# Performance work log

Measured on AMD Instinct MI355X. Metric: run time of the kernel, lower is better.

## Reference

```python
import jax, jax.numpy as jnp
import numpy as np

B, T, C, H = 2, 2048, 1024, 16
D = C // H  # head dim = 64
EPS = 1e-5


def _layernorm(x, g, b):
    mu = jnp.mean(x, axis=-1, keepdims=True)
    var = jnp.mean((x - mu) ** 2, axis=-1, keepdims=True)
    return (x - mu) * jax.lax.rsqrt(var + EPS) * g + b


def setup_inputs() -> dict:
    key = jax.random.key(0)
    ks = jax.random.split(key, 16)
    s = 1.0 / np.sqrt(C)
    inp = {
        "x": jax.random.normal(ks[0], (B, T, C), dtype=jnp.float32),
        "Wq": jax.random.normal(ks[1], (C, C), dtype=jnp.float32) * s,
        "bq": jnp.zeros((C,), jnp.float32),
        "Wk": jax.random.normal(ks[2], (C, C), dtype=jnp.float32) * s,
        "bk": jnp.zeros((C,), jnp.float32),
        "Wv": jax.random.normal(ks[3], (C, C), dtype=jnp.float32) * s,
        "bv": jnp.zeros((C,), jnp.float32),
        "Wo": jax.random.normal(ks[4], (C, C), dtype=jnp.float32) * s,
        "bo": jnp.zeros((C,), jnp.float32),
        "ln1_g": jnp.ones((C,), jnp.float32),
        "ln1_b": jnp.zeros((C,), jnp.float32),
        "ln2_g": jnp.ones((C,), jnp.float32),
        "ln2_b": jnp.zeros((C,), jnp.float32),
        "W1": jax.random.normal(ks[5], (C, 4 * C), dtype=jnp.float32) * s,
        "b1": jnp.zeros((4 * C,), jnp.float32),
        "W2": jax.random.normal(ks[6], (4 * C, C), dtype=jnp.float32) * (1.0 / np.sqrt(4 * C)),
        "b2": jnp.zeros((C,), jnp.float32),
    }
    return inp


def _block(x, Wq, bq, Wk, bk, Wv, bv, Wo, bo, ln1_g, ln1_b, ln2_g, ln2_b, W1, b1, W2, b2):
    # --- attention sublayer (pre-LN, residual) ---
    h = _layernorm(x, ln1_g, ln1_b)
    q = (h @ Wq + bq).reshape(B, T, H, D)
    k = (h @ Wk + bk).reshape(B, T, H, D)
    v = (h @ Wv + bv).reshape(B, T, H, D)
    scores = jnp.einsum("bthd,bshd->bhts", q, k) * (1.0 / np.sqrt(D))
    attn = jax.nn.softmax(scores, axis=-1)  # dropout is identity at eval
    y = jnp.einsum("bhts,bshd->bthd", attn, v).reshape(B, T, C)
    x = x + (y @ Wo + bo)
    # --- MLP sublayer (pre-LN, residual) ---
    h2 = _layernorm(x, ln2_g, ln2_b)
    m = jax.nn.gelu(h2 @ W1 + b1, approximate=False)  # torch nn.GELU() is exact erf
    x = x + (m @ W2 + b2)
    return x


def reference(x, Wq, bq, Wk, bk, Wv, bv, Wo, bo, ln1_g, ln1_b, ln2_g, ln2_b, W1, b1, W2, b2):
    return _block(x, Wq, bq, Wk, bk, Wv, bv, Wo, bo, ln1_g, ln1_b, ln2_g, ln2_b, W1, b1, W2, b2)
```

## Files before the change

kernel.cpp:

```cpp
#include <hip/hip_runtime.h>
#include <math.h>

typedef unsigned short u16;
typedef unsigned int   u32;
using bf16x8 = __attribute__((ext_vector_type(8))) short;
using f32x4  = __attribute__((ext_vector_type(4))) float;
using f32x16 = __attribute__((ext_vector_type(16))) float;

static constexpr int Bb = 2, Tt = 2048, Cc = 1024, Hh = 16, Dd = 64;
static constexpr int QS = 3072;
static constexpr float QSCALE = 0.125f * 1.44269504089f;

__device__ __forceinline__ u16 f2bf(float f){
  u32 u = __builtin_bit_cast(u32, f);
  u += 0x7fffu + ((u >> 16) & 1u);
  return (u16)(u >> 16);
}
__device__ __forceinline__ float bf2f(u16 v){
  u32 u = (u32)v << 16;
  return __builtin_bit_cast(float, u);
}

__device__ __forceinline__ void gl2lds16(const void* g, void* l){
  __builtin_amdgcn_global_load_lds((const __attribute__((address_space(1))) void*)g,
                                   (__attribute__((address_space(3))) void*)l, 16, 0, 0);
}

template<int N> __device__ __forceinline__ void waitvm(){
  if constexpr (N == 0) asm volatile("s_waitcnt vmcnt(0)" ::: "memory");
  else if constexpr (N == 3) asm volatile("s_waitcnt vmcnt(3)" ::: "memory");
  else if constexpr (N == 4) asm volatile("s_waitcnt vmcnt(4)" ::: "memory");
  else if constexpr (N == 6) asm volatile("s_waitcnt vmcnt(6)" ::: "memory");
  else if constexpr (N == 8) asm volatile("s_waitcnt vmcnt(8)" ::: "memory");
}

__device__ __forceinline__ void barrier_pin(){
  __builtin_amdgcn_s_barrier();
  __builtin_amdgcn_sched_barrier(0);
}

__device__ __forceinline__ f32x4 mfma16(bf16x8 a, bf16x8 b, f32x4 c){
  return __builtin_amdgcn_mfma_f32_16x16x32_bf16(a, b, c, 0, 0, 0);
}
__device__ __forceinline__ f32x16 mfma32(bf16x8 a, bf16x8 b, f32x16 c){
  return __builtin_amdgcn_mfma_f32_32x32x16_bf16(a, b, c, 0, 0, 0);
}

__device__ __forceinline__ float exp2f_fast(float x){
#if __has_builtin(__builtin_amdgcn_exp2f)
  return __builtin_amdgcn_exp2f(x);
#else
  return __expf(x * 0.69314718056f);
#endif
}

__device__ __forceinline__ float gelu_f(float x){
  return 0.5f * x * (1.0f + erff(x * 0.70710678118654752f));
}

__device__ __forceinline__ void plane_swap(u32& a, u32& b){
  asm("v_permlane32_swap_b32 %0, %1" : "+v"(a), "+v"(b));
}
__device__ __forceinline__ u32 cvtpk_bf16(float lo, float hi){
  u32 r;
  asm("v_cvt_pk_bf16_f32 %0, %1, %2" : "=v"(r) : "v"(lo), "v"(hi));
  return r;
}

__global__ __launch_bounds__(256) void ln_kernel(const float* __restrict__ x,
    const float* __restrict__ g, const float* __restrict__ b, u16* __restrict__ out)
{
  int row = blockIdx.x;
  int tid = threadIdx.x;
  const float4* xr = (const float4*)(x + (size_t)row * Cc);
  float4 v = xr[tid];
  float s  = v.x + v.y + v.z + v.w;
  float s2 = v.x*v.x + v.y*v.y + v.z*v.z + v.w*v.w;
  #pragma unroll
  for (int off = 1; off < 64; off <<= 1){ s += __shfl_xor(s, off); s2 += __shfl_xor(s2, off); }
  __shared__ float red[8];
  int wid = tid >> 6;
  if ((tid & 63) == 0){ red[wid] = s; red[4 + wid] = s2; }
  __syncthreads();
  s  = red[0] + red[1] + red[2] + red[3];
  s2 = red[4] + red[5] + red[6] + red[7];
  float mu   = s * (1.0f / Cc);
  float var  = s2 * (1.0f / Cc) - mu * mu;
  float rstd = rsqrtf(var + 1e-5f);
  const float4 gg = ((const float4*)g)[tid];
  const float4 bb = ((const float4*)b)[tid];
  ushort4 o;
  o.x = f2bf((v.x - mu) * rstd * gg.x + bb.x);
  o.y = f2bf((v.y - mu) * rstd * gg.y + bb.y);
  o.z = f2bf((v.z - mu) * rstd * gg.z + bb.z);
  o.w = f2bf((v.w - mu) * rstd * gg.w + bb.w);
  *(ushort4*)(out + (size_t)row * Cc + tid * 4) = o;
}

__global__ __launch_bounds__(256) void transpose_cast_kernel(const float* __restrict__ in,
    u16* __restrict__ out, int R, int Ccols)
{
  __shared__ float tile[32][33];
  int tx = threadIdx.x, ty = threadIdx.y;
  int c0 = blockIdx.x * 32, r0 = blockIdx.y * 32;
  #pragma unroll
  for (int j = 0; j < 4; j++) tile[ty + j*8][tx] = in[(size_t)(r0 + ty + j*8) * Ccols + c0 + tx];
  __syncthreads();
  #pragma unroll
  for (int j = 0; j < 4; j++) out[(size_t)(c0 + ty + j*8) * R + r0 + tx] = f2bf(tile[tx][ty + j*8]);
}

__global__ __launch_bounds__(256) void transpose4_kernel(
    const float* __restrict__ s0, const float* __restrict__ s1,
    const float* __restrict__ s2, const float* __restrict__ s3,
    u16* __restrict__ d0, u16* __restrict__ d1, u16* __restrict__ d2, u16* __restrict__ d3)
{
  __shared__ float tile[32][33];
  int z = blockIdx.z;
  const float* in = (z == 0) ? s0 : (z == 1) ? s1 : (z == 2) ? s2 : s3;
  u16* out        = (z == 0) ? d0 : (z == 1) ? d1 : (z == 2) ? d2 : d3;
  int tx = threadIdx.x, ty = threadIdx.y;
  int c0 = blockIdx.x * 32, r0 = blockIdx.y * 32;
  #pragma unroll
  for (int j = 0; j < 4; j++) tile[ty + j*8][tx] = in[(size_t)(r0 + ty + j*8) * 1024 + c0 + tx];
  __syncthreads();
  #pragma unroll
  for (int j = 0; j < 4; j++) out[(size_t)(c0 + ty + j*8) * 1024 + r0 + tx] = f2bf(tile[tx][ty + j*8]);
}

__global__ __launch_bounds__(256) void pack3_kernel(const float* __restrict__ a,
    const float* __restrict__ b, const float* __restrict__ c, float* __restrict__ o)
{
  int i = blockIdx.x * 256 + threadIdx.x;
  float v = (i < 1024) ? a[i] : (i < 2048 ? b[i - 1024] : c[i - 2048]);
  o[i] = v;
}

__global__ __launch_bounds__(256) void transpose_v_kernel(const u16* __restrict__ v, u16* __restrict__ vt)
{
  __shared__ u16 tile[32][33];
  int tx = threadIdx.x, ty = threadIdx.y;
  int bh = blockIdx.z; int b = bh >> 4, h = bh & 15;
  int t0 = blockIdx.x * 32, d0 = blockIdx.y * 32;
  const u16* src = v + (size_t)b * Tt * QS + h * Dd;
  #pragma unroll
  for (int j = 0; j < 4; j++) tile[ty + j*8][tx] = src[(size_t)(t0 + ty + j*8) * QS + d0 + tx];
  __syncthreads();
  u16* dst = vt + (size_t)bh * Dd * Tt;
  #pragma unroll
  for (int j = 0; j < 4; j++) dst[(size_t)(d0 + ty + j*8) * Tt + t0 + tx] = tile[tx][ty + j*8];
}

template<int BM, int BN, int WM, int WN, int WPEU, int EPI>
__global__ __launch_bounds__(WM * WN * 64, WPEU) void gemmc_kernel(
    const u16* __restrict__ A, const u16* __restrict__ BT,
    const float* __restrict__ bias, const float* __restrict__ resid,
    void* __restrict__ out, int K, int ldA, int ldOut)
{
  constexpr int THREADS = WM * WN * 64;
  constexpr int MF = (BM / WM) / 16;
  constexpr int NF = (BN / WN) / 16;
  constexpr int AG = (BM * 4) / THREADS;
  constexpr int BG = (BN * 4) / THREADS;
  constexpr int NLOADS = AG + BG;

  __shared__ alignas(16) u16 As[2][BM * 32];
  __shared__ alignas(16) u16 Bs[2][BN * 32];

  const int tid  = threadIdx.x;
  const int lane = tid & 63, wid = tid >> 6;
  const int l15  = lane & 15, lg = lane >> 4;

  const int gx  = gridDim.x;
  const int lin = blockIdx.x + gx * blockIdx.y;
  const int nwg = gx * gridDim.y;
  const int wl  = (lin & 7) * (nwg >> 3) + (lin >> 3);
  const int rowBase = (wl % gx) * BM, colBase = (wl / gx) * BN;

  const int wr = wid / WN, wc = wid % WN;

  f32x4 acc[MF][NF] = {};

  auto stage = [&](int buf, int k0){
    #pragma unroll
    for (int j = 0; j < AG; j++){
      int g = tid + THREADS * j;
      int row = g >> 2, p = g & 3;
      int w = p ^ (row & 3) ^ ((row >> 2) & 3);
      gl2lds16(A + (size_t)(rowBase + row) * ldA + k0 + w * 8, (u16*)As[buf] + g * 8);
    }
    #pragma unroll
    for (int j = 0; j < BG; j++){
      int g = tid + THREADS * j;
      int row = g >> 2, p = g & 3;
      int w = p ^ (row & 3) ^ ((row >> 2) & 3);
      gl2lds16(BT + (size_t)(colBase + row) * K + k0 + w * 8, (u16*)Bs[buf] + g * 8);
    }
  };

  stage(0, 0);
  const int nt = K >> 5;
  int cur = 0;
  for (int t = 0; t < nt; ++t, cur ^= 1){
    if (t + 1 < nt){ stage(cur ^ 1, (t + 1) << 5); waitvm<NLOADS>(); }
    else           { waitvm<0>(); }
    __builtin_amdgcn_s_barrier();
    __builtin_amdgcn_sched_barrier(0);

    const u16* Asb = (const u16*)As[cur];
    const u16* Bsb = (const u16*)Bs[cur];

    bf16x8 bfr[NF], afr[MF];
    #pragma unroll
    for (int ni = 0; ni < NF; ni++){
      int r = wc * (BN / WN) + ni * 16 + l15;
      bfr[ni] = *(const bf16x8*)(Bsb + r * 32 + ((lg ^ (r & 3) ^ ((r >> 2) & 3)) << 3));
    }
    #pragma unroll
    for (int mi = 0; mi < MF; mi++){
      int r = wr * (BM / WM) + mi * 16 + l15;
      afr[mi] = *(const bf16x8*)(Asb + r * 32 + ((lg ^ (r & 3) ^ ((r >> 2) & 3)) << 3));
    }
    __builtin_amdgcn_s_setprio(1);
    #pragma unroll
    for (int mi = 0; mi < MF; mi++)
      #pragma unroll
      for (int ni = 0; ni < NF; ni++)
        acc[mi][ni] = mfma16(afr[mi], bfr[ni], acc[mi][ni]);
    __builtin_amdgcn_s_setprio(0);

    __builtin_amdgcn_sched_barrier(0);
    __builtin_amdgcn_s_barrier();
  }

  #pragma unroll
  for (int mi = 0; mi < MF; mi++){
    #pragma unroll
    for (int ni = 0; ni < NF; ni++){
      int row = rowBase + wr * (BM / WM) + mi * 16 + lg * 4;
      int col = colBase + wc * (BN / WN) + ni * 16 + l15;
      float bc = bias[col];
      #pragma unroll
      for (int r = 0; r < 4; r++){
        float val = acc[mi][ni][r] + bc;
        size_t idx = (size_t)(row + r) * ldOut + col;
        if constexpr (EPI == 1)      ((float*)out)[idx] = val + resid[idx];
        else if constexpr (EPI == 2) ((u16*)out)[idx]   = f2bf(gelu_f(val));
        else if constexpr (EPI == 3) ((u16*)out)[idx]   = f2bf(col < 1024 ? val * QSCALE : val);
        else                         ((u16*)out)[idx]   = f2bf(val);
      }
    }
  }
}

__global__ __launch_bounds__(256, 4) void attn_kernel(const u16* __restrict__ q, const u16* __restrict__ k,
    const u16* __restrict__ vt, u16* __restrict__ opart, float* __restrict__ ml)
{
  __shared__ alignas(16) u16 Ks[2][64 * 64];
  __shared__ alignas(16) u16 Vs[2][64 * 64];
  int tid  = threadIdx.x;
  int lane = tid & 63, wid = tid >> 6;
  int l31  = lane & 31, hi = lane >> 5;

  int lin = blockIdx.x + 16 * blockIdx.y;
  int wl  = (lin & 7) * 64 + (lin >> 3);
  int qt  = wl & 15, bh = wl >> 4;
  int b = bh >> 4, h = bh & 15;
  int split = blockIdx.z;
  int kt0 = split * (Tt / 2);

  int qglob = qt * 128 + wid * 32 + l31;

  const u16* qp = q + ((size_t)b * Tt + qglob) * QS + h * Dd + hi * 8;
  bf16x8 qf[4];
  #pragma unroll
  for (int s = 0; s < 4; s++) qf[s] = *(const bf16x8*)(qp + s * 16);

  const u16* kbase = k  + (size_t)b * Tt * QS + h * Dd;
  const u16* vbase = vt + (size_t)bh * Dd * Tt;

  f32x16 yacc[2] = {};
  float m2 = -1e30f, lsum = 0.f;

  int g0 = tid, g1 = tid + 256;
  int r0 = g0 >> 3, cb0 = (g0 & 7) ^ (r0 & 7);
  int r1 = g1 >> 3, cb1 = (g1 & 7) ^ (r1 & 7);

  auto stageKV = [&](int buf, int kt){
    gl2lds16(kbase + (size_t)(kt + r0) * QS + cb0 * 8, (u16*)Ks[buf] + wid * 512);
    gl2lds16(kbase + (size_t)(kt + r1) * QS + cb1 * 8, (u16*)Ks[buf] + 2048 + wid * 512);
    gl2lds16(vbase + (size_t)r0 * Tt + kt + cb0 * 8,   (u16*)Vs[buf] + wid * 512);
    gl2lds16(vbase + (size_t)r1 * Tt + kt + cb1 * 8,   (u16*)Vs[buf] + 2048 + wid * 512);
  };

  stageKV(0, kt0);
  int cur = 0;
  for (int kt = kt0; kt < kt0 + Tt / 2; kt += 64) {
    if (kt + 64 < kt0 + Tt / 2) { stageKV(cur ^ 1, kt + 64); waitvm<4>(); }
    else                        { waitvm<0>(); }
    barrier_pin();

    const u16* Ksb = (const u16*)Ks[cur];
    const u16* Vsb = (const u16*)Vs[cur];
    int rx = l31 & 7;

    f32x16 st[2] = {};
    __builtin_amdgcn_s_setprio(1);
    #pragma unroll
    for (int nb = 0; nb < 2; nb++){
      const u16* krow = Ksb + (nb * 32 + l31) * 64;
      #pragma unroll
      for (int s = 0; s < 4; s++){
        bf16x8 kf = *(const bf16x8*)(krow + (((s * 2 + hi) ^ rx) << 3));
        st[nb] = mfma32(kf, qf[s], st[nb]);
      }
    }
    __builtin_amdgcn_s_setprio(0);

    float tm[16];
    #pragma unroll
    for (int i = 0; i < 16; i++) tm[i] = fmaxf(st[0][i], st[1][i]);
    #pragma unroll
    for (int w = 8; w; w >>= 1)
      #pragma unroll
      for (int i = 0; i < w; i++) tm[i] = fmaxf(tm[i], tm[i + w]);
    u32 ma = __builtin_bit_cast(u32, tm[0]), mb = ma;
    plane_swap(ma, mb);
    float mx = fmaxf(__builtin_bit_cast(float, ma), __builtin_bit_cast(float, mb));

    float mnew = fmaxf(m2, mx);
    float alpha = exp2f_fast(m2 - mnew);
    m2 = mnew;

    #pragma unroll
    for (int nb = 0; nb < 2; nb++)
      #pragma unroll
      for (int i = 0; i < 16; i++)
        st[nb][i] = exp2f_fast(st[nb][i] - m2);

    float ts[16];
    #pragma unroll
    for (int i = 0; i < 16; i++) ts[i] = st[0][i] + st[1][i];
    #pragma unroll
    for (int w = 8; w; w >>= 1)
      #pragma unroll
      for (int i = 0; i < w; i++) ts[i] += ts[i + w];
    u32 sa = __builtin_bit_cast(u32, ts[0]), sb = sa;
    plane_swap(sa, sb);
    lsum = lsum * alpha + __builtin_bit_cast(float, sa) + __builtin_bit_cast(float, sb);

    #pragma unroll
    for (int nd = 0; nd < 2; nd++)
      #pragma unroll
      for (int i = 0; i < 16; i++) yacc[nd][i] *= alpha;

    bf16x8 pb[4];
    #pragma unroll
    for (int nb = 0; nb < 2; nb++){
      u32 c[8];
      #pragma unroll
      for (int i = 0; i < 8; i++) c[i] = cvtpk_bf16(st[nb][2 * i], st[nb][2 * i + 1]);
      plane_swap(c[0], c[2]); plane_swap(c[1], c[3]);
      plane_swap(c[4], c[6]); plane_swap(c[5], c[7]);
      u32 f0[4] = {c[0], c[1], c[2], c[3]};
      u32 f1[4] = {c[4], c[5], c[6], c[7]};
      pb[nb * 2 + 0] = *(bf16x8*)f0;
      pb[nb * 2 + 1] = *(bf16x8*)f1;
    }

    __builtin_amdgcn_s_setprio(1);
    #pragma unroll
    for (int nd = 0; nd < 2; nd++){
      const u16* vrow = Vsb + (nd * 32 + l31) * 64;
      #pragma unroll
      for (int ks = 0; ks < 4; ks++){
        bf16x8 vf = *(const bf16x8*)(vrow + (((ks * 2 + hi) ^ rx) << 3));
        yacc[nd] = mfma32(vf, pb[ks], yacc[nd]);
      }
    }
    __builtin_amdgcn_s_setprio(0);

    __builtin_amdgcn_sched_barrier(0);
    barrier_pin();
    cur ^= 1;
  }

  float inv = 1.0f / lsum;
  u16* op = opart + ((size_t)split * (Bb * Tt) + (size_t)b * Tt + qglob) * Cc + h * Dd;
  #pragma unroll
  for (int nd = 0; nd < 2; nd++){
    #pragma unroll
    for (int g = 0; g < 4; g++){
      ushort4 o;
      o.x = f2bf(yacc[nd][g * 4 + 0] * inv);
      o.y = f2bf(yacc[nd][g * 4 + 1] * inv);
      o.z = f2bf(yacc[nd][g * 4 + 2] * inv);
      o.w = f2bf(yacc[nd][g * 4 + 3] * inv);
      *(ushort4*)(op + nd * 32 + g * 8 + hi * 4) = o;
    }
  }
  if (hi == 0){
    float* mlp = ml + (((size_t)split * (Bb * Tt) + (size_t)b * Tt + qglob) * Hh + h) * 2;
    mlp[0] = m2; mlp[1] = lsum;
  }
}

__global__ __launch_bounds__(256) void combine_kernel(const u16* __restrict__ opart,
    const float* __restrict__ ml, u16* __restrict__ y)
{
  int row = blockIdx.x;
  int d0  = threadIdx.x * 4;
  int h   = d0 >> 6;
  const float* p0 = ml + ((size_t)row * Hh + h) * 2;
  const float* p1 = ml + (((size_t)(Bb * Tt) + row) * Hh + h) * 2;
  float m0 = p0[0], l0 = p0[1], m1 = p1[0], l1 = p1[1];
  float M  = fmaxf(m0, m1);
  float u0 = l0 * exp2f_fast(m0 - M), u1 = l1 * exp2f_fast(m1 - M);
  float inv = 1.0f / (u0 + u1);
  float w0 = u0 * inv, w1 = u1 * inv;
  ushort4 a = *(const ushort4*)(opart + (size_t)row * Cc + d0);
  ushort4 c = *(const ushort4*)(opart + ((size_t)(Bb * Tt) + row) * Cc + d0);
  ushort4 o;
  o.x = f2bf(bf2f(a.x) * w0 + bf2f(c.x) * w1);
  o.y = f2bf(bf2f(a.y) * w0 + bf2f(c.y) * w1);
  o.z = f2bf(bf2f(a.z) * w0 + bf2f(c.z) * w1);
  o.w = f2bf(bf2f(a.w) * w0 + bf2f(c.w) * w1);
  *(ushort4*)(y + (size_t)row * Cc + d0) = o;
}

extern "C" void kernel_launch(void* const* d_in, const int* in_sizes, int n_in,
                              void* d_out, int out_size, void* d_ws, size_t ws_size,
                              hipStream_t stream)
{
  (void)in_sizes; (void)n_in; (void)out_size; (void)ws_size;
  const float* x    = (const float*)d_in[0];
  const float* Wq   = (const float*)d_in[1];
  const float* bq   = (const float*)d_in[2];
  const float* Wk   = (const float*)d_in[3];
  const float* bk   = (const float*)d_in[4];
  const float* Wv   = (const float*)d_in[5];
  const float* bv   = (const float*)d_in[6];
  const float* Wo   = (const float*)d_in[7];
  const float* bo   = (const float*)d_in[8];
  const float* ln1g = (const float*)d_in[9];
  const float* ln1b = (const float*)d_in[10];
  const float* ln2g = (const float*)d_in[11];
  const float* ln2b = (const float*)d_in[12];
  const float* W1   = (const float*)d_in[13];
  const float* b1   = (const float*)d_in[14];
  const float* W2   = (const float*)d_in[15];
  const float* b2   = (const float*)d_in[16];

  char* ws = (char*)d_ws;
  const size_t MB = 1024 * 1024;
  u16*   wqkvt = (u16*)(ws + 0 * MB);
  u16*   wot   = (u16*)(ws + 6 * MB);
  u16*   w1t   = (u16*)(ws + 8 * MB);
  u16*   w2t   = (u16*)(ws + 16 * MB);
  float* bqkv  = (float*)(ws + 24 * MB);
  u16*   hbuf  = (u16*)(ws + 25 * MB);
  u16*   qkv   = (u16*)(ws + 33 * MB);
  u16*   vtb   = (u16*)(ws + 57 * MB);
  u16*   yb    = (u16*)(ws + 65 * MB);
  u16*   opart = (u16*)(ws + 73 * MB);
  float* x2    = (float*)(ws + 73 * MB);
  float* mlb   = (float*)(ws + 89 * MB);
  u16*   h2    = hbuf;
  u16*   mb    = qkv;

  dim3 tb(32, 8);
  transpose4_kernel<<<dim3(32, 32, 4), tb, 0, stream>>>(Wq, Wk, Wv, Wo,
      wqkvt, wqkvt + 1024 * 1024, wqkvt + 2048 * 1024, wot);
  transpose_cast_kernel<<<dim3(128, 32), tb, 0, stream>>>(W1, w1t, 1024, 4096);
  transpose_cast_kernel<<<dim3(32, 128), tb, 0, stream>>>(W2, w2t, 4096, 1024);
  pack3_kernel<<<12, 256, 0, stream>>>(bq, bk, bv, bqkv);

  ln_kernel<<<4096, 256, 0, stream>>>(x, ln1g, ln1b, hbuf);

  gemmc_kernel<128, 128, 2, 2, 4, 3><<<dim3(32, 24), 256, 0, stream>>>(hbuf, wqkvt, bqkv, nullptr, qkv, 1024, 1024, 3072);

  transpose_v_kernel<<<dim3(64, 2, 32), tb, 0, stream>>>(qkv + 2048, vtb);

  attn_kernel<<<dim3(16, 32, 2), 256, 0, stream>>>(qkv, qkv + 1024, vtb, opart, mlb);
  combine_kernel<<<4096, 256, 0, stream>>>(opart, mlb, yb);

  gemmc_kernel<64, 128, 2, 2, 4, 1><<<dim3(64, 8), 256, 0, stream>>>(yb, wot, bo, x, x2, 1024, 1024, 1024);

  ln_kernel<<<4096, 256, 0, stream>>>(x2, ln2g, ln2b, h2);

  gemmc_kernel<128, 128, 2, 2, 4, 2><<<dim3(32, 32), 256, 0, stream>>>(h2, w1t, b1, nullptr, mb, 1024, 1024, 4096);

  gemmc_kernel<64, 128, 2, 2, 4, 1><<<dim3(64, 8), 256, 0, stream>>>(mb, w2t, b2, x2, (float*)d_out, 4096, 4096, 1024);
}
```

Measured before the change: 272.7 us.

## Deepen GEMM K-tile to 64 with 8-way swizzle and retune tile shapes

The GEMM kernel now stages 64-wide K slices per iteration instead of 32, using an XOR-by-row&7 LDS swizzle. Global and LDS offsets are precomputed once, and the last iteration is peeled out of the loop. Each GEMM launch also gets new tile sizes: smaller M or N tiles give more workgroups for the QKV, W1, Wo and W2 GEMMs, with occupancy hints adjusted to match. The aim is to halve barrier and sync overhead per K step and improve CU fill, at the cost of more LDS per block and less reuse per tile.

```diff
diff --git a/kernel.cpp b/kernel.cpp
--- a/kernel.cpp
+++ b/kernel.cpp
@@ -28,7 +28,6 @@
 
 template<int N> __device__ __forceinline__ void waitvm(){
   if constexpr (N == 0) asm volatile("s_waitcnt vmcnt(0)" ::: "memory");
-  else if constexpr (N == 3) asm volatile("s_waitcnt vmcnt(3)" ::: "memory");
   else if constexpr (N == 4) asm volatile("s_waitcnt vmcnt(4)" ::: "memory");
   else if constexpr (N == 6) asm volatile("s_waitcnt vmcnt(6)" ::: "memory");
   else if constexpr (N == 8) asm volatile("s_waitcnt vmcnt(8)" ::: "memory");
@@ -66,6 +65,8 @@
   asm("v_cvt_pk_bf16_f32 %0, %1, %2" : "=v"(r) : "v"(lo), "v"(hi));
   return r;
 }
+
+__device__ __forceinline__ bf16x8 ldlds(const u16* p){ return *(const bf16x8*)p; }
 
 __global__ __launch_bounds__(256) void ln_kernel(const float* __restrict__ x,
     const float* __restrict__ g, const float* __restrict__ b, u16* __restrict__ out)
@@ -151,21 +152,20 @@
   for (int j = 0; j < 4; j++) dst[(size_t)(d0 + ty + j*8) * Tt + t0 + tx] = tile[tx][ty + j*8];
 }
 
-template<int BM, int BN, int WM, int WN, int WPEU, int EPI>
-__global__ __launch_bounds__(WM * WN * 64, WPEU) void gemmc_kernel(
+template<int BM, int BN, int WPEU, int EPI>
+__global__ __launch_bounds__(256, WPEU) void gemmc_kernel(
     const u16* __restrict__ A, const u16* __restrict__ BT,
     const float* __restrict__ bias, const float* __restrict__ resid,
     void* __restrict__ out, int K, int ldA, int ldOut)
 {
-  constexpr int THREADS = WM * WN * 64;
-  constexpr int MF = (BM / WM) / 16;
-  constexpr int NF = (BN / WN) / 16;
-  constexpr int AG = (BM * 4) / THREADS;
-  constexpr int BG = (BN * 4) / THREADS;
+  constexpr int MF = BM / 2 / 16;
+  constexpr int NF = BN / 2 / 16;
+  constexpr int AG = BM / 32;
+  constexpr int BG = BN / 32;
   constexpr int NLOADS = AG + BG;
 
-  __shared__ alignas(16) u16 As[2][BM * 32];
-  __shared__ alignas(16) u16 Bs[2][BN * 32];
+  __shared__ alignas(16) u16 As[2][BM * 64];
+  __shared__ alignas(16) u16 Bs[2][BN * 64];
 
   const int tid  = threadIdx.x;
   const int lane = tid & 63, wid = tid >> 6;
@@ -177,68 +177,113 @@
   const int wl  = (lin & 7) * (nwg >> 3) + (lin >> 3);
   const int rowBase = (wl % gx) * BM, colBase = (wl / gx) * BN;
 
-  const int wr = wid / WN, wc = wid % WN;
+  const int wr = wid >> 1, wc = wid & 1;
 
   f32x4 acc[MF][NF] = {};
 
-  auto stage = [&](int buf, int k0){
-    #pragma unroll
-    for (int j = 0; j < AG; j++){
-      int g = tid + THREADS * j;
-      int row = g >> 2, p = g & 3;
-      int w = p ^ (row & 3) ^ ((row >> 2) & 3);
-      gl2lds16(A + (size_t)(rowBase + row) * ldA + k0 + w * 8, (u16*)As[buf] + g * 8);
-    }
-    #pragma unroll
-    for (int j = 0; j < BG; j++){
-      int g = tid + THREADS * j;
-      int row = g >> 2, p = g & 3;
-      int w = p ^ (row & 3) ^ ((row >> 2) & 3);
-      gl2lds16(BT + (size_t)(colBase + row) * K + k0 + w * 8, (u16*)Bs[buf] + g * 8);
-    }
-  };
-
-  stage(0, 0);
-  const int nt = K >> 5;
-  int cur = 0;
-  for (int t = 0; t < nt; ++t, cur ^= 1){
-    if (t + 1 < nt){ stage(cur ^ 1, (t + 1) << 5); waitvm<NLOADS>(); }
-    else           { waitvm<0>(); }
+  const u16* pA[AG];
+  const u16* pB[BG];
+  u32 dA[AG], dB[BG];
+  #pragma unroll
+  for (int j = 0; j < AG; j++){
+    int g = tid + 256 * j;
+    int r = g >> 3, w = (g & 7) ^ (r & 7);
+    pA[j] = A + (size_t)(rowBase + r) * ldA + w * 8;
+    dA[j] = (u32)g * 8;
+  }
+  #pragma unroll
+  for (int j = 0; j < BG; j++){
+    int g = tid + 256 * j;
+    int r = g >> 3, w = (g & 7) ^ (r & 7);
+    pB[j] = BT + (size_t)(colBase + r) * K + w * 8;
+    dB[j] = (u32)g * 8;
+  }
+
+  u32 oa[MF][2], ob[NF][2];
+  #pragma unroll
+  for (int mi = 0; mi < MF; mi++){
+    int r = wr * (BM / 2) + mi * 16 + l15;
+    oa[mi][0] = (u32)(r * 64 + ((lg       ^ (r & 7)) << 3));
+    oa[mi][1] = (u32)(r * 64 + (((4 + lg) ^ (r & 7)) << 3));
+  }
+  #pragma unroll
+  for (int ni = 0; ni < NF; ni++){
+    int r = wc * (BN / 2) + ni * 16 + l15;
+    ob[ni][0] = (u32)(r * 64 + ((lg       ^ (r & 7)) << 3));
+    ob[ni][1] = (u32)(r * 64 + (((4 + lg) ^ (r & 7)) << 3));
+  }
+
+  #pragma unroll
+  for (int j = 0; j < AG; j++){ gl2lds16(pA[j], &As[0][dA[j]]); pA[j] += 64; }
+  #pragma unroll
+  for (int j = 0; j < BG; j++){ gl2lds16(pB[j], &Bs[0][dB[j]]); pB[j] += 64; }
+
+  const int nt = K >> 6;
+  #pragma unroll 2
+  for (int t = 0; t < nt - 1; ++t){
+    const int cur = t & 1, nxt = cur ^ 1;
+    #pragma unroll
+    for (int j = 0; j < AG; j++){ gl2lds16(pA[j], &As[nxt][dA[j]]); pA[j] += 64; }
+    #pragma unroll
+    for (int j = 0; j < BG; j++){ gl2lds16(pB[j], &Bs[nxt][dB[j]]); pB[j] += 64; }
+    waitvm<NLOADS>();
     __builtin_amdgcn_s_barrier();
     __builtin_amdgcn_sched_barrier(0);
 
-    const u16* Asb = (const u16*)As[cur];
-    const u16* Bsb = (const u16*)Bs[cur];
-
-    bf16x8 bfr[NF], afr[MF];
+    bf16x8 afr[MF][2], bfr[NF][2];
+    #pragma unroll
+    for (int mi = 0; mi < MF; mi++){
+      afr[mi][0] = ldlds(&As[cur][oa[mi][0]]);
+      afr[mi][1] = ldlds(&As[cur][oa[mi][1]]);
+    }
     #pragma unroll
     for (int ni = 0; ni < NF; ni++){
-      int r = wc * (BN / WN) + ni * 16 + l15;
-      bfr[ni] = *(const bf16x8*)(Bsb + r * 32 + ((lg ^ (r & 3) ^ ((r >> 2) & 3)) << 3));
-    }
-    #pragma unroll
-    for (int mi = 0; mi < MF; mi++){
-      int r = wr * (BM / WM) + mi * 16 + l15;
-      afr[mi] = *(const bf16x8*)(Asb + r * 32 + ((lg ^ (r & 3) ^ ((r >> 2) & 3)) << 3));
+      bfr[ni][0] = ldlds(&Bs[cur][ob[ni][0]]);
+      bfr[ni][1] = ldlds(&Bs[cur][ob[ni][1]]);
     }
     __builtin_amdgcn_s_setprio(1);
     #pragma unroll
     for (int mi = 0; mi < MF; mi++)
       #pragma unroll
-      for (int ni = 0; ni < NF; ni++)
-        acc[mi][ni] = mfma16(afr[mi], bfr[ni], acc[mi][ni]);
+      for (int ni = 0; ni < NF; ni++){
+        acc[mi][ni] = mfma16(afr[mi][0], bfr[ni][0], acc[mi][ni]);
+        acc[mi][ni] = mfma16(afr[mi][1], bfr[ni][1], acc[mi][ni]);
+      }
     __builtin_amdgcn_s_setprio(0);
 
     __builtin_amdgcn_sched_barrier(0);
     __builtin_amdgcn_s_barrier();
   }
+  {
+    const int cur = (nt - 1) & 1;
+    waitvm<0>();
+    __builtin_amdgcn_s_barrier();
+    bf16x8 afr[MF][2], bfr[NF][2];
+    #pragma unroll
+    for (int mi = 0; mi < MF; mi++){
+      afr[mi][0] = ldlds(&As[cur][oa[mi][0]]);
+      afr[mi][1] = ldlds(&As[cur][oa[mi][1]]);
+    }
+    #pragma unroll
+    for (int ni = 0; ni < NF; ni++){
+      bfr[ni][0] = ldlds(&Bs[cur][ob[ni][0]]);
+      bfr[ni][1] = ldlds(&Bs[cur][ob[ni][1]]);
+    }
+    #pragma unroll
+    for (int mi = 0; mi < MF; mi++)
+      #pragma unroll
+      for (int ni = 0; ni < NF; ni++){
+        acc[mi][ni] = mfma16(afr[mi][0], bfr[ni][0], acc[mi][ni]);
+        acc[mi][ni] = mfma16(afr[mi][1], bfr[ni][1], acc[mi][ni]);
+      }
+  }
 
   #pragma unroll
   for (int mi = 0; mi < MF; mi++){
     #pragma unroll
     for (int ni = 0; ni < NF; ni++){
-      int row = rowBase + wr * (BM / WM) + mi * 16 + lg * 4;
-      int col = colBase + wc * (BN / WN) + ni * 16 + l15;
+      int row = rowBase + wr * (BM / 2) + mi * 16 + lg * 4;
+      int col = colBase + wc * (BN / 2) + ni * 16 + l15;
       float bc = bias[col];
       #pragma unroll
       for (int r = 0; r < 4; r++){
@@ -477,18 +522,18 @@
 
   ln_kernel<<<4096, 256, 0, stream>>>(x, ln1g, ln1b, hbuf);
 
-  gemmc_kernel<128, 128, 2, 2, 4, 3><<<dim3(32, 24), 256, 0, stream>>>(hbuf, wqkvt, bqkv, nullptr, qkv, 1024, 1024, 3072);
+  gemmc_kernel<64, 128, 3, 3><<<dim3(64, 24), 256, 0, stream>>>(hbuf, wqkvt, bqkv, nullptr, qkv, 1024, 1024, 3072);
 
   transpose_v_kernel<<<dim3(64, 2, 32), tb, 0, stream>>>(qkv + 2048, vtb);
 
   attn_kernel<<<dim3(16, 32, 2), 256, 0, stream>>>(qkv, qkv + 1024, vtb, opart, mlb);
   combine_kernel<<<4096, 256, 0, stream>>>(opart, mlb, yb);
 
-  gemmc_kernel<64, 128, 2, 2, 4, 1><<<dim3(64, 8), 256, 0, stream>>>(yb, wot, bo, x, x2, 1024, 1024, 1024);
+  gemmc_kernel<64, 64, 4, 1><<<dim3(64, 16), 256, 0, stream>>>(yb, wot, bo, x, x2, 1024, 1024, 1024);
 
   ln_kernel<<<4096, 256, 0, stream>>>(x2, ln2g, ln2b, h2);
 
-  gemmc_kernel<128, 128, 2, 2, 4, 2><<<dim3(32, 32), 256, 0, stream>>>(h2, w1t, b1, nullptr, mb, 1024, 1024, 4096);
-
-  gemmc_kernel<64, 128, 2, 2, 4, 1><<<dim3(64, 8), 256, 0, stream>>>(mb, w2t, b2, x2, (float*)d_out, 4096, 4096, 1024);
-}
+  gemmc_kernel<64, 128, 3, 2><<<dim3(64, 32), 256, 0, stream>>>(h2, w1t, b1, nullptr, mb, 1024, 1024, 4096);
+
+  gemmc_kernel<64, 64, 4, 1><<<dim3(64, 16), 256, 0, stream>>>(mb, w2t, b2, x2, (float*)d_out, 4096, 4096, 1024);
+}
```

Measured after the change: 258.3 us. 5.3% less time.
